# Optimization experiments

Hardware: AMD Instinct MI355X
Metric: run time of the kernel (lower is better)

The kernel has to match this reference:

```python
import jax, jax.numpy as jnp
import numpy as np

B, S, D, H = 2, 2048, 1024, 16
HD = D // H  # head_dim = 64
ROPE_BASE = 10000.0
NEG_MIN = jnp.finfo(jnp.float32).min


def _rope_cos_sin(seq_len, head_dim):
    inv_freq = 1.0 / (ROPE_BASE ** (jnp.arange(0, head_dim, 2, dtype=jnp.float32) / head_dim))
    t = jnp.arange(seq_len, dtype=jnp.float32)
    freqs = jnp.einsum('i,j->ij', t, inv_freq)           # [S, HD/2]
    emb = jnp.concatenate([freqs, freqs], axis=-1)        # [S, HD]
    return jnp.cos(emb), jnp.sin(emb)


def _rotate_half(x):
    x1, x2 = jnp.split(x, 2, axis=-1)
    return jnp.concatenate([-x2, x1], axis=-1)


def setup_inputs() -> dict:
    key = jax.random.key(0)
    ks = jax.random.split(key, 5)
    sc = 0.02
    hidden_states = jax.random.normal(ks[0], (B, S, D), dtype=jnp.float32)
    wq = jax.random.normal(ks[1], (D, D), dtype=jnp.float32) * sc
    wk = jax.random.normal(ks[2], (D, D), dtype=jnp.float32) * sc
    wv = jax.random.normal(ks[3], (D, D), dtype=jnp.float32) * sc
    wo = jax.random.normal(ks[4], (D, D), dtype=jnp.float32) * sc
    # additive causal mask [B,1,S,S]: 0 on/below diagonal, large negative above
    causal = jnp.tril(jnp.ones((S, S), dtype=jnp.bool_))
    attention_mask = jnp.where(causal, 0.0, NEG_MIN)[None, None, :, :].astype(jnp.float32)
    attention_mask = jnp.broadcast_to(attention_mask, (B, 1, S, S))
    position_ids = jnp.broadcast_to(jnp.arange(S, dtype=jnp.int32)[None, :], (B, S))
    return {"hidden_states": hidden_states, "attention_mask": attention_mask,
            "wq": wq, "wk": wk, "wv": wv, "wo": wo, "position_ids": position_ids}


def reference(hidden_states, attention_mask, wq, wk, wv, wo, position_ids):
    bsz, q_len, _ = hidden_states.shape

    def shape_heads(x):
        return x.reshape(bsz, q_len, H, HD).transpose(0, 2, 1, 3)  # [B,H,S,HD]

    q = shape_heads(hidden_states @ wq)
    k = shape_heads(hidden_states @ wk)
    v = shape_heads(hidden_states @ wv)

    cos, sin = _rope_cos_sin(q_len, HD)                   # [S, HD]
    cos = cos[position_ids][:, None, :, :]                # [B,1,S,HD]
    sin = sin[position_ids][:, None, :, :]
    q = q * cos + _rotate_half(q) * sin
    k = k * cos + _rotate_half(k) * sin

    scores = jnp.einsum('bhqd,bhkd->bhqk', q, k) / jnp.sqrt(jnp.float32(HD))
    scores = jnp.maximum(scores + attention_mask, NEG_MIN)
    attn = jax.nn.softmax(scores, axis=-1)
    out = jnp.einsum('bhqk,bhkd->bhqd', attn, v)          # [B,H,S,HD]
    out = out.transpose(0, 2, 1, 3).reshape(bsz, q_len, D)
    return out @ wo
```

## Files before the change

kernel.cpp:

```cpp
#include <hip/hip_runtime.h>
#include <hip/hip_bf16.h>

#define B_ 2
#define S_ 2048
#define D_ 1024
#define H_ 16
#define HD_ 64

typedef unsigned short u16;
typedef __attribute__((ext_vector_type(8))) short short8;
typedef __attribute__((ext_vector_type(4))) float f32x4;

#if __has_builtin(__builtin_amdgcn_exp2f)
#define EXP2F(x) __builtin_amdgcn_exp2f(x)
#else
#define EXP2F(x) exp2f(x)
#endif

__device__ __forceinline__ u16 f2bf(float f) {
  union { float f; unsigned u; } v; v.f = f;
  unsigned r = v.u + 0x7fffu + ((v.u >> 16) & 1u);
  return (u16)(r >> 16);
}
__device__ __forceinline__ unsigned pkbf(float a, float b) {
  union { __hip_bfloat162 h; unsigned u; } v;
  v.h = __float22bfloat162_rn(float2{a, b});
  return v.u;
}
__device__ __forceinline__ void gload_lds16(const u16* g, u16* l) {
  __builtin_amdgcn_global_load_lds((const __attribute__((address_space(1))) void*)g,
                                   (__attribute__((address_space(3))) void*)l, 16, 0, 0);
}

__global__ __launch_bounds__(256) void prep_kernel(const float* __restrict__ hs,
                                                   const float* __restrict__ W0,
                                                   const float* __restrict__ W1,
                                                   const float* __restrict__ W2,
                                                   const float* __restrict__ W3,
                                                   u16* __restrict__ Xb,
                                                   u16* __restrict__ WT) {
  __shared__ float T[64][65];
  if (blockIdx.z == 4) {
    const int base = (blockIdx.y * 16 + blockIdx.x) * 4096 + threadIdx.x;
#pragma unroll 4
    for (int i = 0; i < 16; ++i) {
      const int idx = base + i * 256;
      const float4 v = ((const float4*)hs)[idx];
      ushort4 o;
      o.x = f2bf(v.x); o.y = f2bf(v.y); o.z = f2bf(v.z); o.w = f2bf(v.w);
      ((ushort4*)Xb)[idx] = o;
    }
    return;
  }
  const float* Wz[4] = {W0, W1, W2, W3};
  const float* W = Wz[blockIdx.z];
  u16* dst = WT + (size_t)blockIdx.z * (1024 * 1024);
  const int nb = blockIdx.x * 64, kb = blockIdx.y * 64;
  const int t = threadIdx.x;
  const int r = t >> 2, c4 = (t & 3) * 16;
#pragma unroll
  for (int i = 0; i < 4; ++i) {
    float4 v = *(const float4*)&W[(kb + r) * D_ + nb + c4 + i * 4];
    T[r][c4 + i * 4 + 0] = v.x;
    T[r][c4 + i * 4 + 1] = v.y;
    T[r][c4 + i * 4 + 2] = v.z;
    T[r][c4 + i * 4 + 3] = v.w;
  }
  __syncthreads();
#pragma unroll
  for (int i = 0; i < 4; ++i) {
    ushort4 o;
    o.x = f2bf(T[c4 + i * 4 + 0][r]);
    o.y = f2bf(T[c4 + i * 4 + 1][r]);
    o.z = f2bf(T[c4 + i * 4 + 2][r]);
    o.w = f2bf(T[c4 + i * 4 + 3][r]);
    *(ushort4*)&dst[(nb + r) * D_ + kb + c4 + i * 4] = o;
  }
}

template <int BN, int MODE, int DB>
__global__ __launch_bounds__(256) void gemm_kernel(const u16* __restrict__ A,
                                                   const u16* __restrict__ BT,
                                                   float* __restrict__ out0,
                                                   u16* __restrict__ oQ,
                                                   u16* __restrict__ oK,
                                                   u16* __restrict__ oV,
                                                   const int* __restrict__ posarr) {
  constexpr int K = D_;
  constexpr int NT = BN / 32;
  constexpr int BI = BN / 32;
  constexpr int ABANK = 128 * 64;
  constexpr int BBANK = BN * 64;
  constexpr int STAGE = (DB + 1) * (ABANK + BBANK);
  constexpr int EPIU = (MODE == 1) ? 128 * 136 : 0;
  constexpr int SMU = STAGE > EPIU ? STAGE : EPIU;
  __shared__ u16 smem[SMU];
  u16* AsP = smem;
  u16* BsP = smem + (DB + 1) * ABANK;

  const int t = threadIdx.x, lane = t & 63, w = t >> 6;
  const int l15 = lane & 15, quad = lane >> 4;
  const int n0 = blockIdx.x * BN, m0 = blockIdx.y * 128;
  const int wm = (w >> 1) * 64, wn = (w & 1) * (BN / 2);

  f32x4 acc[4][NT];
#pragma unroll
  for (int mt = 0; mt < 4; ++mt)
#pragma unroll
    for (int nt = 0; nt < NT; ++nt) acc[mt][nt] = (f32x4){0.f, 0.f, 0.f, 0.f};

  const u16* ag[4]; int aoff[4];
  const u16* bg[BI]; int boff[BI];
#pragma unroll
  for (int j = 0; j < 4; ++j) {
    int slot = w * 256 + j * 64 + lane;
    int row = slot >> 3, q = (slot & 7) ^ (row & 7);
    ag[j] = A + (size_t)(m0 + row) * K + q * 8;
    aoff[j] = (w * 256 + j * 64) * 8;
  }
#pragma unroll
  for (int j = 0; j < BI; ++j) {
    int slot = w * (BI * 64) + j * 64 + lane;
    int row = slot >> 3, q = (slot & 7) ^ (row & 7);
    bg[j] = BT + (size_t)(n0 + row) * K + q * 8;
    boff[j] = (w * (BI * 64) + j * 64) * 8;
  }

  auto stage = [&](int k0, int buf) {
#pragma unroll
    for (int j = 0; j < 4; ++j) gload_lds16(ag[j] + k0, AsP + buf * ABANK + aoff[j]);
#pragma unroll
    for (int j = 0; j < BI; ++j) gload_lds16(bg[j] + k0, BsP + buf * BBANK + boff[j]);
  };
  auto compute = [&](int buf) {
    const u16* Ab = AsP + buf * ABANK;
    const u16* Bb = BsP + buf * BBANK;
#pragma unroll
    for (int kc = 0; kc < 2; ++kc) {
      short8 af[4], bf[NT];
#pragma unroll
      for (int mt = 0; mt < 4; ++mt) {
        int row = wm + mt * 16 + l15;
        af[mt] = *(const short8*)&Ab[row * 64 + (((kc * 4 + quad) ^ (row & 7)) * 8)];
      }
#pragma unroll
      for (int nt = 0; nt < NT; ++nt) {
        int col = wn + nt * 16 + l15;
        bf[nt] = *(const short8*)&Bb[col * 64 + (((kc * 4 + quad) ^ (col & 7)) * 8)];
      }
#pragma unroll
      for (int mt = 0; mt < 4; ++mt)
#pragma unroll
        for (int nt = 0; nt < NT; ++nt)
          acc[mt][nt] = __builtin_amdgcn_mfma_f32_16x16x32_bf16(af[mt], bf[nt], acc[mt][nt], 0, 0, 0);
    }
  };

  if constexpr (DB == 0) {
    for (int k0 = 0; k0 < K; k0 += 64) {
      __syncthreads();
      stage(k0, 0);
      __syncthreads();
      compute(0);
    }
  } else {
    stage(0, 0);
#pragma unroll 1
    for (int it = 0; it < K / 64; ++it) {
      __syncthreads();
      if (it + 1 < K / 64) stage((it + 1) * 64, (it + 1) & 1);
      compute(it & 1);
    }
  }

  if (MODE == 0) {
#pragma unroll
    for (int mt = 0; mt < 4; ++mt) {
      const int row0 = m0 + wm + mt * 16 + quad * 4;
#pragma unroll
      for (int nt = 0; nt < NT; ++nt) {
        const int col = n0 + wn + nt * 16 + l15;
#pragma unroll
        for (int r = 0; r < 4; ++r) out0[(size_t)(row0 + r) * 1024 + col] = acc[mt][nt][r];
      }
    }
  } else {
    const int widx = n0 >> 10;
    if (widx == 2) {
      __syncthreads();
      u16* Epi = smem;
#pragma unroll
      for (int nt = 0; nt < NT; ++nt) {
        const int col = wn + nt * 16 + l15;
#pragma unroll
        for (int mt = 0; mt < 4; ++mt) {
          const int row0 = wm + mt * 16 + quad * 4;
          uint2 pk;
          pk.x = pkbf(acc[mt][nt][0], acc[mt][nt][1]);
          pk.y = pkbf(acc[mt][nt][2], acc[mt][nt][3]);
          *(uint2*)&Epi[col * 136 + row0] = pk;
        }
      }
      __syncthreads();
      const int col = t >> 1, half = t & 1;
      const int cc = (n0 + col) & 1023;
      const int h = cc >> 6, d = cc & 63;
      const int bb = m0 >> 11;
      const int s0 = (m0 & (S_ - 1)) + half * 64;
      u16* gp = oV + ((((size_t)(bb * H_ + h) * HD_ + d)) << 11) + s0;
#pragma unroll
      for (int i = 0; i < 8; ++i)
        ((uint4*)gp)[i] = *(const uint4*)&Epi[col * 136 + half * 64 + i * 8];
    } else {
      u16* dst = (widx == 0) ? oQ : oK;
      const float scale = (widx == 0) ? 0.18033688011f : 1.0f;
      float invf[2];
      invf[0] = exp2f(-0.41524101186f * (float)l15);
      invf[1] = exp2f(-0.41524101186f * (float)(16 + l15));
      __syncthreads();
      u16* Epi = smem;
#pragma unroll
      for (int mt = 0; mt < 4; ++mt) {
        const int lrow0 = wm + mt * 16 + quad * 4;
#pragma unroll
        for (int r = 0; r < 4; ++r) {
          const int rw = m0 + lrow0 + r;
          const int b = rw >> 11, s = rw & (S_ - 1);
          const float pos = (float)posarr[b * S_ + s];
#pragma unroll
          for (int nt2 = 0; nt2 < 2; ++nt2) {
            float sn, c;
            __sincosf(pos * invf[nt2], &sn, &c);
            const float x1 = acc[mt][nt2][r], x2 = acc[mt][nt2 + 2][r];
            const int d = nt2 * 16 + l15;
            Epi[(lrow0 + r) * 136 + wn + d] = f2bf((x1 * c - x2 * sn) * scale);
            Epi[(lrow0 + r) * 136 + wn + d + 32] = f2bf((x2 * c + x1 * sn) * scale);
          }
        }
      }
      __syncthreads();
      const int bb = m0 >> 11, s0 = m0 & (S_ - 1);
      const int sl = t >> 1, d0 = (t & 1) * 32;
#pragma unroll
      for (int hh = 0; hh < 2; ++hh) {
        const int h = ((n0 + hh * 64) & 1023) >> 6;
        u16* gp = dst + (((size_t)(bb * H_ + h) * S_ + s0 + sl) << 6) + d0;
#pragma unroll
        for (int k2 = 0; k2 < 4; ++k2)
          ((uint4*)gp)[k2] = *(const uint4*)&Epi[sl * 136 + hh * 64 + d0 + k2 * 8];
      }
    }
  }
}

__global__ __launch_bounds__(256, 2) void attn_kernel(const u16* __restrict__ Q,
                                                      const u16* __restrict__ Kx,
                                                      const u16* __restrict__ Vt,
                                                      u16* __restrict__ AO) {
  __shared__ u16 Ks[2][512 * 8];
  __shared__ u16 Vs[2][512 * 8];
  __shared__ u16 Pw[4][128 * 8];
  const int t = threadIdx.x;
  const int lane = t & 63, w = t >> 6;
  const int l15 = lane & 15, quad = lane >> 4;
  const int idx = blockIdx.x;
  const int pr = (idx >> 3) & 15;
  const int bh = (idx & 7) | ((idx >> 7) << 3);
  const int qtA = pr, qtB = 31 - pr;
  const u16* qp = Q + bh * (S_ * HD_);
  const u16* kp = Kx + bh * (S_ * HD_);
  const u16* vp = Vt + bh * (HD_ * S_);
  const int wq16 = w * 16;
  const int q_loA = qtA * 64 + wq16;
  const int q_loB = qtB * 64 + wq16;

  int srow[2], sq[2];
#pragma unroll
  for (int jj = 0; jj < 2; ++jj) {
    int slot = w * 128 + jj * 64 + lane;
    srow[jj] = slot >> 3;
    sq[jj] = (slot & 7) ^ (srow[jj] & 7);
  }
  auto stage = [&](int kt, int buf) {
#pragma unroll
    for (int jj = 0; jj < 2; ++jj)
      gload_lds16(kp + (size_t)(kt * 64 + srow[jj]) * 64 + sq[jj] * 8,
                  &Ks[buf][(w * 128 + jj * 64) * 8]);
#pragma unroll
    for (int jj = 0; jj < 2; ++jj)
      gload_lds16(vp + (size_t)srow[jj] * S_ + kt * 64 + sq[jj] * 8,
                  &Vs[buf][(w * 128 + jj * 64) * 8]);
  };

  short8 qfA[2], qfB[2];
#pragma unroll
  for (int kc = 0; kc < 2; ++kc) {
    qfA[kc] = *(const short8*)&qp[(q_loA + l15) * HD_ + kc * 32 + quad * 8];
    qfB[kc] = *(const short8*)&qp[(q_loB + l15) * HD_ + kc * 32 + quad * 8];
  }

  f32x4 oA[4], oB[4];
  float mA = -INFINITY, lA = 0.f, mB = -INFINITY, lB = 0.f;
#pragma unroll
  for (int i = 0; i < 4; ++i) {
    oA[i] = (f32x4){0.f, 0.f, 0.f, 0.f};
    oB[i] = (f32x4){0.f, 0.f, 0.f, 0.f};
  }

  auto chainStep = [&](bool diag, const short8* qf, const short8* kf, const short8* vf,
                       f32x4* o, float& m_, float& l_) {
    f32x4 sa[4];
#pragma unroll
    for (int i = 0; i < 4; ++i) sa[i] = (f32x4){0.f, 0.f, 0.f, 0.f};
#pragma unroll
    for (int kc = 0; kc < 2; ++kc)
#pragma unroll
      for (int nt = 0; nt < 4; ++nt)
        sa[nt] = __builtin_amdgcn_mfma_f32_16x16x32_bf16(kf[kc * 4 + nt], qf[kc], sa[nt], 0, 0, 0);
    if (diag) {
#pragma unroll
      for (int nt = 0; nt < 4; ++nt)
#pragma unroll
        for (int r = 0; r < 4; ++r)
          if (nt * 16 + quad * 4 + r > wq16 + l15) sa[nt][r] = -INFINITY;
    }
    float mx = -INFINITY;
#pragma unroll
    for (int nt = 0; nt < 4; ++nt)
#pragma unroll
      for (int r = 0; r < 4; ++r) mx = fmaxf(mx, sa[nt][r]);
    mx = fmaxf(mx, __shfl_xor(mx, 16));
    mx = fmaxf(mx, __shfl_xor(mx, 32));
    const float mn = fmaxf(m_, mx);
    const float alpha = EXP2F(m_ - mn);
    m_ = mn;
    float p[16];
    float sum = 0.f;
#pragma unroll
    for (int nt = 0; nt < 4; ++nt)
#pragma unroll
      for (int r = 0; r < 4; ++r) {
        const float pe = EXP2F(sa[nt][r] - mn);
        p[nt * 4 + r] = pe;
        sum += pe;
      }
    sum += __shfl_xor(sum, 16);
    sum += __shfl_xor(sum, 32);
    l_ = l_ * alpha + sum;
#pragma unroll
    for (int dt = 0; dt < 4; ++dt)
#pragma unroll
      for (int r = 0; r < 4; ++r) o[dt][r] *= alpha;
#pragma unroll
    for (int nt = 0; nt < 4; ++nt) {
      const int q = nt * 2 + (quad >> 1);
      uint2 pk;
      pk.x = pkbf(p[nt * 4 + 0], p[nt * 4 + 1]);
      pk.y = pkbf(p[nt * 4 + 2], p[nt * 4 + 3]);
      *(uint2*)&Pw[w][(l15 * 8 + (q ^ (l15 & 7))) * 8 + (quad & 1) * 4] = pk;
    }
#pragma unroll
    for (int kc = 0; kc < 2; ++kc) {
      short8 pf = *(const short8*)&Pw[w][(l15 * 8 + (((kc * 4) + quad) ^ (l15 & 7))) * 8];
#pragma unroll
      for (int dt = 0; dt < 4; ++dt)
        o[dt] = __builtin_amdgcn_mfma_f32_16x16x32_bf16(vf[dt * 2 + kc], pf, o[dt], 0, 0, 0);
    }
  };

  const int ktmax = qtB;
  stage(0, 0);
#pragma unroll 1
  for (int kt = 0; kt <= ktmax; ++kt) {
    __syncthreads();
    if (kt < ktmax) stage(kt + 1, (kt + 1) & 1);
    const int buf = kt & 1;
    short8 kf[8], vf[8];
#pragma unroll
    for (int kc = 0; kc < 2; ++kc)
#pragma unroll
      for (int nt = 0; nt < 4; ++nt) {
        const int row = nt * 16 + l15;
        kf[kc * 4 + nt] =
            *(const short8*)&Ks[buf][(row * 8 + ((kc * 4 + quad) ^ (row & 7))) * 8];
      }
#pragma unroll
    for (int dt = 0; dt < 4; ++dt)
#pragma unroll
      for (int kc = 0; kc < 2; ++kc) {
        const int row = dt * 16 + l15;
        vf[dt * 2 + kc] =
            *(const short8*)&Vs[buf][(row * 8 + ((kc * 4 + quad) ^ (row & 7))) * 8];
      }
    chainStep(kt == qtB, qfB, kf, vf, oB, mB, lB);
    if (kt <= qtA) chainStep(kt == qtA, qfA, kf, vf, oA, mA, lA);
  }

  const int b = bh >> 4, h = bh & 15;
  const float liA = 1.0f / lA, liB = 1.0f / lB;
  const size_t baseA = ((size_t)(b * S_ + q_loA + l15)) * D_ + h * HD_;
  const size_t baseB = ((size_t)(b * S_ + q_loB + l15)) * D_ + h * HD_;
#pragma unroll
  for (int dt = 0; dt < 4; ++dt)
#pragma unroll
    for (int rr = 0; rr < 2; ++rr) {
      *(unsigned*)&AO[baseA + dt * 16 + quad * 4 + rr * 2] =
          pkbf(oA[dt][rr * 2] * liA, oA[dt][rr * 2 + 1] * liA);
      *(unsigned*)&AO[baseB + dt * 16 + quad * 4 + rr * 2] =
          pkbf(oB[dt][rr * 2] * liB, oB[dt][rr * 2 + 1] * liB);
    }
}

extern "C" void kernel_launch(void* const* d_in, const int* in_sizes, int n_in,
                              void* d_out, int out_size, void* d_ws, size_t ws_size,
                              hipStream_t stream) {
  const float* hs = (const float*)d_in[0];
  const float* wq = (const float*)d_in[2];
  const float* wk = (const float*)d_in[3];
  const float* wv = (const float*)d_in[4];
  const float* wo = (const float*)d_in[5];
  const int* pos = (const int*)d_in[6];
  float* out = (float*)d_out;

  char* ws = (char*)d_ws;
  const size_t MB = (size_t)1 << 20;
  u16* Xb = (u16*)(ws);
  u16* WT = (u16*)(ws + 8 * MB);
  u16* Qh = (u16*)(ws + 16 * MB);
  u16* Kh = (u16*)(ws + 24 * MB);
  u16* Vt = (u16*)(ws + 32 * MB);
  u16* AO = (u16*)(ws + 40 * MB);

  prep_kernel<<<dim3(16, 16, 5), 256, 0, stream>>>(hs, wq, wk, wv, wo, Xb, WT);

  gemm_kernel<128, 1, 0><<<dim3(24, 32), 256, 0, stream>>>(Xb, WT, nullptr, Qh, Kh, Vt, pos);

  attn_kernel<<<512, 256, 0, stream>>>(Qh, Kh, Vt, AO);

  gemm_kernel<64, 0, 1><<<dim3(16, 32), 256, 0, stream>>>(AO, WT + 3 * 1024 * 1024, out,
                                                          nullptr, nullptr, nullptr, nullptr);
}
```

Baseline: 210.4 us.

## Remap GEMM blocks per XCD and stage two KV tiles per attention barrier

GEMM launches become 1D, and block indices are remapped so that each XCD (selected by blockIdx mod 8) owns four adjacent 128-row M-tiles and walks the N tiles, aiming for better L2 reuse of A rows within a chiplet. The attention kernel now stages two 64-key K/V tiles per double-buffer slot and processes both between syncthreads, halving barrier count. LDS use for K/V doubles to 64KB, which may reduce occupancy below the two blocks requested in launch bounds.

```diff
diff --git a/kernel.cpp b/kernel.cpp
--- a/kernel.cpp
+++ b/kernel.cpp
@@ -100,7 +100,10 @@
 
   const int t = threadIdx.x, lane = t & 63, w = t >> 6;
   const int l15 = lane & 15, quad = lane >> 4;
-  const int n0 = blockIdx.x * BN, m0 = blockIdx.y * 128;
+  const int flat = blockIdx.x;
+  const int xcd = flat & 7, j = flat >> 3;
+  const int m0 = ((xcd << 2) + (j & 3)) * 128;
+  const int n0 = (j >> 2) * BN;
   const int wm = (w >> 1) * 64, wn = (w & 1) * (BN / 2);
 
   f32x4 acc[4][NT];
@@ -112,25 +115,25 @@
   const u16* ag[4]; int aoff[4];
   const u16* bg[BI]; int boff[BI];
 #pragma unroll
-  for (int j = 0; j < 4; ++j) {
-    int slot = w * 256 + j * 64 + lane;
+  for (int jj = 0; jj < 4; ++jj) {
+    int slot = w * 256 + jj * 64 + lane;
     int row = slot >> 3, q = (slot & 7) ^ (row & 7);
-    ag[j] = A + (size_t)(m0 + row) * K + q * 8;
-    aoff[j] = (w * 256 + j * 64) * 8;
-  }
-#pragma unroll
-  for (int j = 0; j < BI; ++j) {
-    int slot = w * (BI * 64) + j * 64 + lane;
+    ag[jj] = A + (size_t)(m0 + row) * K + q * 8;
+    aoff[jj] = (w * 256 + jj * 64) * 8;
+  }
+#pragma unroll
+  for (int jj = 0; jj < BI; ++jj) {
+    int slot = w * (BI * 64) + jj * 64 + lane;
     int row = slot >> 3, q = (slot & 7) ^ (row & 7);
-    bg[j] = BT + (size_t)(n0 + row) * K + q * 8;
-    boff[j] = (w * (BI * 64) + j * 64) * 8;
+    bg[jj] = BT + (size_t)(n0 + row) * K + q * 8;
+    boff[jj] = (w * (BI * 64) + jj * 64) * 8;
   }
 
   auto stage = [&](int k0, int buf) {
 #pragma unroll
-    for (int j = 0; j < 4; ++j) gload_lds16(ag[j] + k0, AsP + buf * ABANK + aoff[j]);
-#pragma unroll
-    for (int j = 0; j < BI; ++j) gload_lds16(bg[j] + k0, BsP + buf * BBANK + boff[j]);
+    for (int jj = 0; jj < 4; ++jj) gload_lds16(ag[jj] + k0, AsP + buf * ABANK + aoff[jj]);
+#pragma unroll
+    for (int jj = 0; jj < BI; ++jj) gload_lds16(bg[jj] + k0, BsP + buf * BBANK + boff[jj]);
   };
   auto compute = [&](int buf) {
     const u16* Ab = AsP + buf * ABANK;
@@ -257,8 +260,8 @@
                                                       const u16* __restrict__ Kx,
                                                       const u16* __restrict__ Vt,
                                                       u16* __restrict__ AO) {
-  __shared__ u16 Ks[2][512 * 8];
-  __shared__ u16 Vs[2][512 * 8];
+  __shared__ u16 Ks[2][2][512 * 8];
+  __shared__ u16 Vs[2][2][512 * 8];
   __shared__ u16 Pw[4][128 * 8];
   const int t = threadIdx.x;
   const int lane = t & 63, w = t >> 6;
@@ -281,15 +284,20 @@
     srow[jj] = slot >> 3;
     sq[jj] = (slot & 7) ^ (srow[jj] & 7);
   }
-  auto stage = [&](int kt, int buf) {
+  auto stageT = [&](int kt, int buf, int tt) {
 #pragma unroll
     for (int jj = 0; jj < 2; ++jj)
       gload_lds16(kp + (size_t)(kt * 64 + srow[jj]) * 64 + sq[jj] * 8,
-                  &Ks[buf][(w * 128 + jj * 64) * 8]);
+                  &Ks[buf][tt][(w * 128 + jj * 64) * 8]);
 #pragma unroll
     for (int jj = 0; jj < 2; ++jj)
       gload_lds16(vp + (size_t)srow[jj] * S_ + kt * 64 + sq[jj] * 8,
-                  &Vs[buf][(w * 128 + jj * 64) * 8]);
+                  &Vs[buf][tt][(w * 128 + jj * 64) * 8]);
+  };
+  auto stageGroup = [&](int g, int buf, int ktmax) {
+    const int kt0 = g * 2;
+    stageT(kt0, buf, 0);
+    if (kt0 + 1 <= ktmax) stageT(kt0 + 1, buf, 1);
   };
 
   short8 qfA[2], qfB[2];
@@ -368,21 +376,14 @@
     }
   };
 
-  const int ktmax = qtB;
-  stage(0, 0);
-#pragma unroll 1
-  for (int kt = 0; kt <= ktmax; ++kt) {
-    __syncthreads();
-    if (kt < ktmax) stage(kt + 1, (kt + 1) & 1);
-    const int buf = kt & 1;
-    short8 kf[8], vf[8];
+  auto loadFrags = [&](int buf, int tt, short8* kf, short8* vf) {
 #pragma unroll
     for (int kc = 0; kc < 2; ++kc)
 #pragma unroll
       for (int nt = 0; nt < 4; ++nt) {
         const int row = nt * 16 + l15;
         kf[kc * 4 + nt] =
-            *(const short8*)&Ks[buf][(row * 8 + ((kc * 4 + quad) ^ (row & 7))) * 8];
+            *(const short8*)&Ks[buf][tt][(row * 8 + ((kc * 4 + quad) ^ (row & 7))) * 8];
       }
 #pragma unroll
     for (int dt = 0; dt < 4; ++dt)
@@ -390,10 +391,28 @@
       for (int kc = 0; kc < 2; ++kc) {
         const int row = dt * 16 + l15;
         vf[dt * 2 + kc] =
-            *(const short8*)&Vs[buf][(row * 8 + ((kc * 4 + quad) ^ (row & 7))) * 8];
-      }
-    chainStep(kt == qtB, qfB, kf, vf, oB, mB, lB);
-    if (kt <= qtA) chainStep(kt == qtA, qfA, kf, vf, oA, mA, lA);
+            *(const short8*)&Vs[buf][tt][(row * 8 + ((kc * 4 + quad) ^ (row & 7))) * 8];
+      }
+  };
+
+  const int ktmax = qtB;
+  const int ngroups = (ktmax + 2) >> 1;
+  short8 kf[8], vf[8];
+  stageGroup(0, 0, ktmax);
+#pragma unroll 1
+  for (int g = 0; g < ngroups; ++g) {
+    __syncthreads();
+    if (g + 1 < ngroups) stageGroup(g + 1, (g + 1) & 1, ktmax);
+    const int buf = g & 1;
+    const int kt0 = 2 * g;
+    loadFrags(buf, 0, kf, vf);
+    chainStep(kt0 == qtB, qfB, kf, vf, oB, mB, lB);
+    if (kt0 <= qtA) chainStep(kt0 == qtA, qfA, kf, vf, oA, mA, lA);
+    if (kt0 + 1 <= ktmax) {
+      loadFrags(buf, 1, kf, vf);
+      chainStep(kt0 + 1 == qtB, qfB, kf, vf, oB, mB, lB);
+      if (kt0 + 1 <= qtA) chainStep(kt0 + 1 == qtA, qfA, kf, vf, oA, mA, lA);
+    }
   }
 
   const int b = bh >> 4, h = bh & 15;
@@ -433,10 +452,10 @@
 
   prep_kernel<<<dim3(16, 16, 5), 256, 0, stream>>>(hs, wq, wk, wv, wo, Xb, WT);
 
-  gemm_kernel<128, 1, 0><<<dim3(24, 32), 256, 0, stream>>>(Xb, WT, nullptr, Qh, Kh, Vt, pos);
+  gemm_kernel<128, 1, 0><<<768, 256, 0, stream>>>(Xb, WT, nullptr, Qh, Kh, Vt, pos);
 
   attn_kernel<<<512, 256, 0, stream>>>(Qh, Kh, Vt, AO);
 
-  gemm_kernel<64, 0, 1><<<dim3(16, 32), 256, 0, stream>>>(AO, WT + 3 * 1024 * 1024, out,
-                                                          nullptr, nullptr, nullptr, nullptr);
-}
+  gemm_kernel<64, 0, 1><<<512, 256, 0, stream>>>(AO, WT + 3 * 1024 * 1024, out,
+                                                 nullptr, nullptr, nullptr, nullptr);
+}
```

Measured after the change: 206.0 us. 2.1% less time.
